# Performance work log

Measured on AMD Instinct MI355X. Metric: run time of the kernel, lower is better.

## Reference

```python
import jax, jax.numpy as jnp
import numpy as np

N, E, D_IN, HID, HEADS = 50000, 800000, 128, 32, 8
NEG_SLOPE = 0.2


def gat_conv(x, src, dst, W_src, W_dst, a_src, a_dst, b, heads, ch, concat):
    n = x.shape[0]
    hs = (x @ W_src).reshape(n, heads, ch)  # source-side features [N,H,C]
    hd = (x @ W_dst).reshape(n, heads, ch)  # dest-side features   [N,H,C]
    alpha_s = jnp.einsum('nhc,hc->nh', hs, a_src)  # [N,H]
    alpha_d = jnp.einsum('nhc,hc->nh', hd, a_dst)  # [N,H]
    e = jax.nn.leaky_relu(alpha_s[src] + alpha_d[dst], NEG_SLOPE)  # [E,H]
    # segment softmax over edges grouped by destination node
    m = jax.ops.segment_max(e, dst, num_segments=n)
    m = jnp.where(jnp.isfinite(m), m, 0.0)
    e = jnp.exp(e - jax.lax.stop_gradient(m)[dst])
    denom = jax.ops.segment_sum(e, dst, num_segments=n)
    alpha = e / (denom[dst] + 1e-16)  # [E,H]
    # weighted scatter-aggregate of source features to destinations
    out = jax.ops.segment_sum(hs[src] * alpha[:, :, None], dst, num_segments=n)  # [N,H,C]
    out = out.reshape(n, heads * ch) if concat else out.mean(axis=1)
    return out + b


def setup_inputs() -> dict:
    key = jax.random.key(0)
    ks = jax.random.split(key, 12)
    glorot = lambda k, shape: jax.random.normal(k, shape, jnp.float32) * np.sqrt(2.0 / (shape[0] + shape[-1]))
    x = jax.random.normal(ks[0], (N, D_IN), jnp.float32)
    edge_index = jax.random.randint(ks[1], (2, E), 0, N, jnp.int64)
    return {
        'x': x,
        'edge_index': edge_index,
        'W1_src': glorot(ks[2], (D_IN, HEADS * HID)),
        'W1_dst': glorot(ks[3], (D_IN, HEADS * HID)),
        'a1_src': glorot(ks[4], (HEADS, HID)),
        'a1_dst': glorot(ks[5], (HEADS, HID)),
        'b1': jnp.zeros((HEADS * HID,), jnp.float32),
        'W2_src': glorot(ks[6], (HEADS * HID, HID)),
        'W2_dst': glorot(ks[7], (HEADS * HID, HID)),
        'a2_src': glorot(ks[8], (1, HID)),
        'a2_dst': glorot(ks[9], (1, HID)),
        'b2': jnp.zeros((HID,), jnp.float32),
    }


def reference(x, edge_index, W1_src, W1_dst, a1_src, a1_dst, b1,
              W2_src, W2_dst, a2_src, a2_dst, b2):
    src, dst = edge_index[0], edge_index[1]
    h = gat_conv(x, src, dst, W1_src, W1_dst, a1_src, a1_dst, b1, HEADS, HID, True)
    h = jax.nn.relu(h)
    out = gat_conv(h, src, dst, W2_src, W2_dst, a2_src, a2_dst, b2, 1, HID, True)
    return out
```

## Files before the change

### kernel.cpp

```cpp
#include <hip/hip_runtime.h>
#include <hip/hip_bf16.h>

#define NEG_SLOPE 0.2f

typedef unsigned int uint;
typedef unsigned short ushort;
typedef __attribute__((ext_vector_type(8))) short short8;
typedef __attribute__((ext_vector_type(4))) float floatx4;

static __device__ __forceinline__ ushort f2bf(float f) {
    uint u = __float_as_uint(f);
    uint r = (u + 0x7fffu + ((u >> 16) & 1u)) >> 16;
    return (ushort)r;
}
static __device__ __forceinline__ float bf2f(uint s) {
    return __uint_as_float(s << 16);
}

__global__ __launch_bounds__(256) void histprep_kernel(
    const int* __restrict__ dst, int* __restrict__ deg, int E, int HB,
    const float* __restrict__ W1_src, const float* __restrict__ W2_src,
    const float* __restrict__ W1_dst, const float* __restrict__ a1_dst,
    const float* __restrict__ W2_dst, const float* __restrict__ a2_dst,
    ushort* __restrict__ W1t, ushort* __restrict__ W2t,
    float* __restrict__ wc1, float* __restrict__ wc2) {
    if (blockIdx.x < (uint)HB) {
        int i = blockIdx.x * blockDim.x + threadIdx.x;
        int e0 = i * 2;
        if (e0 + 1 < E) {
            int2 d2 = ((const int2*)dst)[i];
            atomicAdd(&deg[d2.x], 1);
            atomicAdd(&deg[d2.y], 1);
        } else if (e0 < E) {
            atomicAdd(&deg[dst[e0]], 1);
        }
        return;
    }
    int i = (blockIdx.x - HB) * blockDim.x + threadIdx.x;
    if (i < 32768) {
        int nc = i & 255, k = i >> 8;
        W1t[nc * 128 + k] = f2bf(W1_src[k * 256 + nc]);
    } else if (i < 32768 + 8192) {
        int i2 = i - 32768;
        int c = i2 & 31, k = i2 >> 5;
        W2t[c * 256 + k] = f2bf(W2_src[k * 32 + c]);
    } else if (i < 32768 + 8192 + 1024) {
        int i3 = i - 32768 - 8192;
        int k = i3 >> 3, h = i3 & 7;
        float s = 0.f;
#pragma unroll
        for (int c = 0; c < 32; ++c)
            s += W1_dst[k * 256 + h * 32 + c] * a1_dst[h * 32 + c];
        wc1[i3] = s;
    } else if (i < 32768 + 8192 + 1024 + 256) {
        int k = i - 32768 - 8192 - 1024;
        float s = 0.f;
#pragma unroll
        for (int c = 0; c < 32; ++c)
            s += W2_dst[k * 32 + c] * a2_dst[c];
        wc2[k] = s;
    }
}

__global__ __launch_bounds__(256) void scanrs_kernel(
    const int* __restrict__ deg, int* __restrict__ rs,
    int* __restrict__ cursor, int* __restrict__ agg,
    int* __restrict__ flag, int n, int E) {
    __shared__ int sh[256];
    int tid = threadIdx.x;
    int c = blockIdx.x;
    int i = c * 256 + tid;
    int d = (i < n) ? deg[i] : 0;
    sh[tid] = d;
    __syncthreads();
    for (int off = 1; off < 256; off <<= 1) {
        int t = (tid >= off) ? sh[tid - off] : 0;
        __syncthreads();
        sh[tid] += t;
        __syncthreads();
    }
    int incl = sh[tid];
    if (tid == 255) {
        agg[c] = incl;
        __threadfence();
        __hip_atomic_store(&flag[c], 1, __ATOMIC_RELEASE,
                           __HIP_MEMORY_SCOPE_AGENT);
    }
    int vt = 0;
    if (tid < c) {
        while (__hip_atomic_load(&flag[tid], __ATOMIC_ACQUIRE,
                                 __HIP_MEMORY_SCOPE_AGENT) == 0) {}
        vt = agg[tid];
    }
    __syncthreads();
    sh[tid] = vt;
    __syncthreads();
    for (int off = 128; off > 0; off >>= 1) {
        if (tid < off) sh[tid] += sh[tid + off];
        __syncthreads();
    }
    int boff = sh[0];
    if (i < n) {
        int v = incl - d + boff;
        rs[i] = v;
        cursor[i] = v;
    }
    if (c == 0 && tid == 0) rs[n] = E;
}

__global__ __launch_bounds__(256) void fill_kernel(
    const int* __restrict__ src, const int* __restrict__ dst,
    int* __restrict__ cursor, int* __restrict__ csr_src, int E) {
    int i = blockIdx.x * blockDim.x + threadIdx.x;
    int e0 = i * 2;
    if (e0 + 1 < E) {
        int2 d2 = ((const int2*)dst)[i];
        int2 s2 = ((const int2*)src)[i];
        int p0 = atomicAdd(&cursor[d2.x], 1);
        int p1 = atomicAdd(&cursor[d2.y], 1);
        csr_src[p0] = s2.x;
        csr_src[p1] = s2.y;
    } else if (e0 < E) {
        int pos = atomicAdd(&cursor[dst[e0]], 1);
        csr_src[pos] = src[e0];
    }
}

__global__ __launch_bounds__(256) void gemm1_mfma(
    const float* __restrict__ x, const ushort* __restrict__ W1t,
    const float* __restrict__ a_src, const float* __restrict__ wc1,
    ushort* __restrict__ hs1b, float* __restrict__ as1,
    float* __restrict__ ad1, int n) {
    __shared__ ushort At[128 * 128];
    __shared__ ushort Out[128 * 128];
    int m0 = blockIdx.x * 128;
    int tid = threadIdx.x;
#pragma unroll
    for (int i = 0; i < 8; ++i) {
        int id = tid + i * 256;
        int m = id >> 4, c = id & 15;
        int gm = m0 + m;
        uint4 pk = {0, 0, 0, 0};
        if (gm < n) {
            const float4* xp = (const float4*)(x + (size_t)gm * 128 + c * 8);
            float4 v0 = xp[0], v1 = xp[1];
            pk.x = (uint)f2bf(v0.x) | ((uint)f2bf(v0.y) << 16);
            pk.y = (uint)f2bf(v0.z) | ((uint)f2bf(v0.w) << 16);
            pk.z = (uint)f2bf(v1.x) | ((uint)f2bf(v1.y) << 16);
            pk.w = (uint)f2bf(v1.z) | ((uint)f2bf(v1.w) << 16);
        }
        *(uint4*)(At + m * 128 + ((c ^ (m & 15)) * 8)) = pk;
    }
    __syncthreads();
    int wid = tid >> 6, lane = tid & 63;
    int q = lane >> 4, l16 = lane & 15;
    int wm = (wid >> 1) * 64;
    int wn = (wid & 1) * 64;
    floatx4 z = {0.f, 0.f, 0.f, 0.f};
    for (int nhalf = 0; nhalf < 2; ++nhalf) {
        int gn0 = nhalf * 128 + wn;
        floatx4 acc[4][4];
#pragma unroll
        for (int mt = 0; mt < 4; ++mt)
#pragma unroll
            for (int nt = 0; nt < 4; ++nt) acc[mt][nt] = z;
#pragma unroll
        for (int s = 0; s < 4; ++s) {
            short8 af[4], bf[4];
#pragma unroll
            for (int mt = 0; mt < 4; ++mt) {
                int row = wm + mt * 16 + l16;
                int c = s * 4 + q;
                af[mt] = *(const short8*)(At + row * 128 + ((c ^ (row & 15)) * 8));
            }
#pragma unroll
            for (int nt = 0; nt < 4; ++nt) {
                int col = gn0 + nt * 16 + l16;
                bf[nt] = *(const short8*)(W1t + col * 128 + s * 32 + q * 8);
            }
#pragma unroll
            for (int mt = 0; mt < 4; ++mt)
#pragma unroll
                for (int nt = 0; nt < 4; ++nt)
                    acc[mt][nt] = __builtin_amdgcn_mfma_f32_16x16x32_bf16(
                        af[mt], bf[nt], acc[mt][nt], 0, 0, 0);
        }
        __syncthreads();
#pragma unroll
        for (int mt = 0; mt < 4; ++mt)
#pragma unroll
            for (int nt = 0; nt < 4; ++nt) {
                floatx4 a = acc[mt][nt];
                int colL = wn + nt * 16 + l16;
#pragma unroll
                for (int r = 0; r < 4; ++r) {
                    int rowL = wm + mt * 16 + q * 4 + r;
                    Out[rowL * 128 + colL] = f2bf(a[r]);
                }
            }
        __syncthreads();
#pragma unroll
        for (int i = 0; i < 8; ++i) {
            int id = tid + i * 256;
            int m = id >> 4, c8 = id & 15;
            int gm = m0 + m;
            if (gm < n) {
                uint4 v = *(uint4*)(Out + m * 128 + c8 * 8);
                *(uint4*)(hs1b + (size_t)gm * 256 + nhalf * 128 + c8 * 8) = v;
            }
        }
#pragma unroll
        for (int i = 0; i < 2; ++i) {
            int id = tid + i * 256;
            int m = id & 127, hl = id >> 7;
            int gm = m0 + m;
            if (gm < n) {
                int h = nhalf * 4 + hl;
                const ushort* row = Out + m * 128 + hl * 32;
                const float* av = a_src + h * 32;
                float s = 0.f;
#pragma unroll
                for (int c = 0; c < 32; ++c) s += bf2f(row[c]) * av[c];
                as1[(size_t)gm * 8 + h] = s;
            }
        }
    }
#pragma unroll
    for (int i = 0; i < 4; ++i) {
        int id = tid + i * 256;
        int m = id & 127, h = id >> 7;
        int gm = m0 + m;
        if (gm < n) {
            float s = 0.f;
            for (int c = 0; c < 16; ++c) {
                const ushort* p = At + m * 128 + ((c ^ (m & 15)) * 8);
#pragma unroll
                for (int jj = 0; jj < 8; ++jj)
                    s += bf2f(p[jj]) * wc1[(c * 8 + jj) * 8 + h];
            }
            ad1[(size_t)gm * 8 + h] = s;
        }
    }
}

__global__ __launch_bounds__(256) void gather1(
    const int* __restrict__ csr_src, const int* __restrict__ rs,
    const ushort* __restrict__ hs1b, const float* __restrict__ as1,
    const float* __restrict__ ad1, const float* __restrict__ b1,
    ushort* __restrict__ h1b, int n) {
    int gid = blockIdx.x * blockDim.x + threadIdx.x;
    int node = gid >> 6;
    int lane = threadIdx.x & 63;
    if (node >= n) return;
    int j = lane >> 5, l = lane & 31;
    int h = l >> 2;
    float ad_v = ad1[node * 8 + h];
    int start = rs[node], cnt = rs[node + 1] - start;
    float acc0 = 0.f, acc1 = 0.f, acc2 = 0.f, acc3 = 0.f;
    float acc4 = 0.f, acc5 = 0.f, acc6 = 0.f, acc7 = 0.f;
    float dacc = 0.f;
    int i = j;
    for (; i + 2 < cnt; i += 4) {
        int sA = csr_src[start + i];
        int sB = csr_src[start + i + 2];
        float tA = as1[sA * 8 + h] + ad_v;
        float tB = as1[sB * 8 + h] + ad_v;
        uint4 vA = *(const uint4*)(hs1b + (size_t)sA * 256 + l * 8);
        uint4 vB = *(const uint4*)(hs1b + (size_t)sB * 256 + l * 8);
        tA = (tA >= 0.f) ? tA : NEG_SLOPE * tA;
        tB = (tB >= 0.f) ? tB : NEG_SLOPE * tB;
        float wA = __expf(tA);
        float wB = __expf(tB);
        acc0 += bf2f(vA.x & 0xffffu) * wA + bf2f(vB.x & 0xffffu) * wB;
        acc1 += bf2f(vA.x >> 16) * wA + bf2f(vB.x >> 16) * wB;
        acc2 += bf2f(vA.y & 0xffffu) * wA + bf2f(vB.y & 0xffffu) * wB;
        acc3 += bf2f(vA.y >> 16) * wA + bf2f(vB.y >> 16) * wB;
        acc4 += bf2f(vA.z & 0xffffu) * wA + bf2f(vB.z & 0xffffu) * wB;
        acc5 += bf2f(vA.z >> 16) * wA + bf2f(vB.z >> 16) * wB;
        acc6 += bf2f(vA.w & 0xffffu) * wA + bf2f(vB.w & 0xffffu) * wB;
        acc7 += bf2f(vA.w >> 16) * wA + bf2f(vB.w >> 16) * wB;
        dacc += wA + wB;
    }
    for (; i < cnt; i += 2) {
        int s = csr_src[start + i];
        float t = as1[s * 8 + h] + ad_v;
        uint4 v = *(const uint4*)(hs1b + (size_t)s * 256 + l * 8);
        t = (t >= 0.f) ? t : NEG_SLOPE * t;
        float w = __expf(t);
        acc0 += bf2f(v.x & 0xffffu) * w;
        acc1 += bf2f(v.x >> 16) * w;
        acc2 += bf2f(v.y & 0xffffu) * w;
        acc3 += bf2f(v.y >> 16) * w;
        acc4 += bf2f(v.z & 0xffffu) * w;
        acc5 += bf2f(v.z >> 16) * w;
        acc6 += bf2f(v.w & 0xffffu) * w;
        acc7 += bf2f(v.w >> 16) * w;
        dacc += w;
    }
    acc0 += __shfl_xor(acc0, 32, 64);
    acc1 += __shfl_xor(acc1, 32, 64);
    acc2 += __shfl_xor(acc2, 32, 64);
    acc3 += __shfl_xor(acc3, 32, 64);
    acc4 += __shfl_xor(acc4, 32, 64);
    acc5 += __shfl_xor(acc5, 32, 64);
    acc6 += __shfl_xor(acc6, 32, 64);
    acc7 += __shfl_xor(acc7, 32, 64);
    dacc += __shfl_xor(dacc, 32, 64);
    if (j == 0) {
        float inv = 1.f / (dacc + 1e-16f);
        float4 b0 = ((const float4*)b1)[l * 2];
        float4 b4 = ((const float4*)b1)[l * 2 + 1];
        float o0 = fmaxf(fmaf(acc0, inv, b0.x), 0.f);
        float o1 = fmaxf(fmaf(acc1, inv, b0.y), 0.f);
        float o2 = fmaxf(fmaf(acc2, inv, b0.z), 0.f);
        float o3 = fmaxf(fmaf(acc3, inv, b0.w), 0.f);
        float o4 = fmaxf(fmaf(acc4, inv, b4.x), 0.f);
        float o5 = fmaxf(fmaf(acc5, inv, b4.y), 0.f);
        float o6 = fmaxf(fmaf(acc6, inv, b4.z), 0.f);
        float o7 = fmaxf(fmaf(acc7, inv, b4.w), 0.f);
        uint4 pk;
        pk.x = (uint)f2bf(o0) | ((uint)f2bf(o1) << 16);
        pk.y = (uint)f2bf(o2) | ((uint)f2bf(o3) << 16);
        pk.z = (uint)f2bf(o4) | ((uint)f2bf(o5) << 16);
        pk.w = (uint)f2bf(o6) | ((uint)f2bf(o7) << 16);
        *(uint4*)(h1b + (size_t)node * 256 + l * 8) = pk;
    }
}

__global__ __launch_bounds__(256) void gemm2_mfma(
    const ushort* __restrict__ h1b, const ushort* __restrict__ W2t,
    const float* __restrict__ a2_src, const float* __restrict__ wc2,
    ushort* __restrict__ hs2b, float* __restrict__ as2,
    float* __restrict__ ad2, int n) {
    __shared__ ushort At[128 * 256];
    __shared__ ushort Out[128 * 32];
    int m0 = blockIdx.x * 128;
    int tid = threadIdx.x;
#pragma unroll
    for (int i = 0; i < 16; ++i) {
        int id = tid + i * 256;
        int m = id >> 5, c = id & 31;
        int gm = m0 + m;
        uint4 v = {0, 0, 0, 0};
        if (gm < n) v = *(const uint4*)(h1b + (size_t)gm * 256 + c * 8);
        *(uint4*)(At + m * 256 + ((c ^ (m & 15)) * 8)) = v;
    }
    __syncthreads();
    int wid = tid >> 6, lane = tid & 63;
    int q = lane >> 4, l16 = lane & 15;
    int wm = wid * 32;
    floatx4 z = {0.f, 0.f, 0.f, 0.f};
    floatx4 acc[2][2] = {{z, z}, {z, z}};
#pragma unroll
    for (int s = 0; s < 8; ++s) {
        short8 af[2], bf[2];
#pragma unroll
        for (int mt = 0; mt < 2; ++mt) {
            int row = wm + mt * 16 + l16;
            int c = s * 4 + q;
            af[mt] = *(const short8*)(At + row * 256 + ((c ^ (row & 15)) * 8));
        }
#pragma unroll
        for (int nt = 0; nt < 2; ++nt) {
            int col = nt * 16 + l16;
            bf[nt] = *(const short8*)(W2t + col * 256 + s * 32 + q * 8);
        }
#pragma unroll
        for (int mt = 0; mt < 2; ++mt)
#pragma unroll
            for (int nt = 0; nt < 2; ++nt)
                acc[mt][nt] = __builtin_amdgcn_mfma_f32_16x16x32_bf16(
                    af[mt], bf[nt], acc[mt][nt], 0, 0, 0);
    }
#pragma unroll
    for (int mt = 0; mt < 2; ++mt)
#pragma unroll
        for (int nt = 0; nt < 2; ++nt) {
            floatx4 a = acc[mt][nt];
            int colL = nt * 16 + l16;
#pragma unroll
            for (int r = 0; r < 4; ++r) {
                int rowL = wm + mt * 16 + q * 4 + r;
                Out[rowL * 32 + colL] = f2bf(a[r]);
            }
        }
    __syncthreads();
#pragma unroll
    for (int i = 0; i < 2; ++i) {
        int id = tid + i * 256;
        int c4 = id & 3, m = id >> 2;
        int gm = m0 + m;
        if (gm < n)
            *(uint4*)(hs2b + (size_t)gm * 32 + c4 * 8) =
                *(uint4*)(Out + m * 32 + c4 * 8);
    }
    if (tid < 128) {
        int gm = m0 + tid;
        if (gm < n) {
            float s = 0.f;
#pragma unroll
            for (int c2 = 0; c2 < 32; ++c2)
                s += bf2f(Out[tid * 32 + c2]) * a2_src[c2];
            as2[gm] = s;
        }
    } else {
        int m = tid - 128, gm = m0 + m;
        if (gm < n) {
            float s = 0.f;
            for (int c = 0; c < 32; ++c) {
                const ushort* p = At + m * 256 + ((c ^ (m & 15)) * 8);
#pragma unroll
                for (int jj = 0; jj < 8; ++jj)
                    s += bf2f(p[jj]) * wc2[c * 8 + jj];
            }
            ad2[gm] = s;
        }
    }
}

__global__ __launch_bounds__(256) void gather2(
    const int* __restrict__ csr_src, const int* __restrict__ rs,
    const ushort* __restrict__ hs2b, const float* __restrict__ as2,
    const float* __restrict__ ad2, const float* __restrict__ b2,
    float* __restrict__ out, int n) {
    int gid = blockIdx.x * blockDim.x + threadIdx.x;
    int node = gid >> 6;
    int lane = threadIdx.x & 63;
    if (node >= n) return;
    int g = lane >> 3, l = lane & 7;
    float ad_v = ad2[node];
    int start = rs[node], cnt = rs[node + 1] - start;
    float a0 = 0.f, a1 = 0.f, a2 = 0.f, a3 = 0.f, dacc = 0.f;
    for (int i = g; i < cnt; i += 8) {
        int s = csr_src[start + i];
        float t = as2[s] + ad_v;
        t = (t >= 0.f) ? t : NEG_SLOPE * t;
        float w = __expf(t);
        uint2 v = *(const uint2*)(hs2b + (size_t)s * 32 + l * 4);
        a0 += bf2f(v.x & 0xffffu) * w;
        a1 += bf2f(v.x >> 16) * w;
        a2 += bf2f(v.y & 0xffffu) * w;
        a3 += bf2f(v.y >> 16) * w;
        dacc += w;
    }
#pragma unroll
    for (int m = 8; m <= 32; m <<= 1) {
        a0 += __shfl_xor(a0, m, 64);
        a1 += __shfl_xor(a1, m, 64);
        a2 += __shfl_xor(a2, m, 64);
        a3 += __shfl_xor(a3, m, 64);
        dacc += __shfl_xor(dacc, m, 64);
    }
    if (g == 0) {
        float inv = 1.f / (dacc + 1e-16f);
        float4 bv = ((const float4*)b2)[l];
        float4 o;
        o.x = fmaf(a0, inv, bv.x);
        o.y = fmaf(a1, inv, bv.y);
        o.z = fmaf(a2, inv, bv.z);
        o.w = fmaf(a3, inv, bv.w);
        *(float4*)(out + (size_t)node * 32 + l * 4) = o;
    }
}

extern "C" void kernel_launch(void* const* d_in, const int* in_sizes, int n_in,
                              void* d_out, int out_size, void* d_ws, size_t ws_size,
                              hipStream_t stream) {
    const float* x      = (const float*)d_in[0];
    const int*   eidx   = (const int*)d_in[1];
    const float* W1_src = (const float*)d_in[2];
    const float* W1_dst = (const float*)d_in[3];
    const float* a1_src = (const float*)d_in[4];
    const float* a1_dst = (const float*)d_in[5];
    const float* b1     = (const float*)d_in[6];
    const float* W2_src = (const float*)d_in[7];
    const float* W2_dst = (const float*)d_in[8];
    const float* a2_src = (const float*)d_in[9];
    const float* a2_dst = (const float*)d_in[10];
    const float* b2     = (const float*)d_in[11];

    const int n = in_sizes[0] / 128;
    const int E = in_sizes[1] / 2;
    const int* srcp = eidx;
    const int* dstp = eidx + E;
    const int nb = (n + 255) / 256;

    char* ws = (char*)d_ws;
    size_t o = 0;
    auto alloc = [&](size_t bytes) {
        void* p = ws + o;
        o += (bytes + 255) & ~(size_t)255;
        return p;
    };
    ushort* W1t  = (ushort*)alloc(256 * 128 * 2);
    ushort* W2t  = (ushort*)alloc(32 * 256 * 2);
    ushort* hs1b = (ushort*)alloc((size_t)n * 256 * 2);
    ushort* h1b  = (ushort*)alloc((size_t)n * 256 * 2);
    ushort* hs2b = (ushort*)alloc((size_t)n * 32 * 2);
    float* as1 = (float*)alloc((size_t)n * 8 * 4);
    float* ad1 = (float*)alloc((size_t)n * 8 * 4);
    float* as2 = (float*)alloc((size_t)n * 4);
    float* ad2 = (float*)alloc((size_t)n * 4);
    float* wc1 = (float*)alloc(1024 * 4);
    float* wc2 = (float*)alloc(256 * 4);
    int* csrmeta = (int*)alloc(((size_t)n + 512) * 4);
    int* deg  = csrmeta;
    int* agg  = csrmeta + n;
    int* flag = csrmeta + n + 256;
    int* rs      = (int*)alloc(((size_t)n + 1) * 4);
    int* cursor  = (int*)alloc((size_t)n * 4);
    int* csr_src = (int*)alloc((size_t)E * 4);

    hipMemsetAsync(csrmeta, 0, ((size_t)n + 512) * sizeof(int), stream);

    const int HB = (E / 2 + 255) / 256;
    const int PB = (32768 + 8192 + 1024 + 256 + 255) / 256;
    histprep_kernel<<<HB + PB, 256, 0, stream>>>(
        dstp, deg, E, HB, W1_src, W2_src, W1_dst, a1_dst, W2_dst, a2_dst,
        W1t, W2t, wc1, wc2);
    scanrs_kernel<<<nb, 256, 0, stream>>>(deg, rs, cursor, agg, flag, n, E);
    fill_kernel<<<(E / 2 + 255) / 256, 256, 0, stream>>>(srcp, dstp, cursor,
                                                         csr_src, E);

    gemm1_mfma<<<(n + 127) / 128, 256, 0, stream>>>(
        x, W1t, a1_src, wc1, hs1b, as1, ad1, n);
    gather1<<<(n + 3) / 4, 256, 0, stream>>>(
        csr_src, rs, hs1b, as1, ad1, b1, h1b, n);

    gemm2_mfma<<<(n + 127) / 128, 256, 0, stream>>>(
        h1b, W2t, a2_src, wc2, hs2b, as2, ad2, n);
    gather2<<<(n + 3) / 4, 256, 0, stream>>>(
        csr_src, rs, hs2b, as2, ad2, b2, (float*)d_out, n);
}
```

Baseline: 323.4 us.

## Fold attention projections into GEMM weights and split gemm1 over column halves

```diff
diff --git a/kernel.cpp b/kernel.cpp
--- a/kernel.cpp
+++ b/kernel.cpp
@@ -19,11 +19,11 @@
 
 __global__ __launch_bounds__(256) void histprep_kernel(
     const int* __restrict__ dst, int* __restrict__ deg, int E, int HB,
-    const float* __restrict__ W1_src, const float* __restrict__ W2_src,
+    const float* __restrict__ W1_src, const float* __restrict__ a1_src,
     const float* __restrict__ W1_dst, const float* __restrict__ a1_dst,
+    const float* __restrict__ W2_src, const float* __restrict__ a2_src,
     const float* __restrict__ W2_dst, const float* __restrict__ a2_dst,
-    ushort* __restrict__ W1t, ushort* __restrict__ W2t,
-    float* __restrict__ wc1, float* __restrict__ wc2) {
+    ushort* __restrict__ W1e, ushort* __restrict__ W2e) {
     if (blockIdx.x < (uint)HB) {
         int i = blockIdx.x * blockDim.x + threadIdx.x;
         int e0 = i * 2;
@@ -39,26 +39,35 @@
     int i = (blockIdx.x - HB) * blockDim.x + threadIdx.x;
     if (i < 32768) {
         int nc = i & 255, k = i >> 8;
-        W1t[nc * 128 + k] = f2bf(W1_src[k * 256 + nc]);
-    } else if (i < 32768 + 8192) {
-        int i2 = i - 32768;
-        int c = i2 & 31, k = i2 >> 5;
-        W2t[c * 256 + k] = f2bf(W2_src[k * 32 + c]);
-    } else if (i < 32768 + 8192 + 1024) {
-        int i3 = i - 32768 - 8192;
-        int k = i3 >> 3, h = i3 & 7;
+        W1e[nc * 128 + k] = f2bf(W1_src[k * 256 + nc]);
+    } else if (i < 34816) {
+        int j = i - 32768;
+        int h = (j >> 7) & 7, k = j & 127;
+        bool is_ws = j < 1024;
+        const float* W = is_ws ? W1_src : W1_dst;
+        const float* a = is_ws ? a1_src : a1_dst;
         float s = 0.f;
 #pragma unroll
         for (int c = 0; c < 32; ++c)
-            s += W1_dst[k * 256 + h * 32 + c] * a1_dst[h * 32 + c];
-        wc1[i3] = s;
-    } else if (i < 32768 + 8192 + 1024 + 256) {
-        int k = i - 32768 - 8192 - 1024;
+            s += W[k * 256 + h * 32 + c] * a[h * 32 + c];
+        W1e[((is_ws ? 256 : 264) + h) * 128 + k] = f2bf(s);
+    } else if (i < 34816 + 8192) {
+        int j = i - 34816;
+        int c = j & 31, k = j >> 5;
+        W2e[c * 256 + k] = f2bf(W2_src[k * 32 + c]);
+    } else if (i < 34816 + 8192 + 512) {
+        int j = i - 34816 - 8192;
+        int k = j & 255;
+        bool is_ws = j < 256;
+        const float* W = is_ws ? W2_src : W2_dst;
+        const float* a = is_ws ? a2_src : a2_dst;
         float s = 0.f;
 #pragma unroll
-        for (int c = 0; c < 32; ++c)
-            s += W2_dst[k * 32 + c] * a2_dst[c];
-        wc2[k] = s;
+        for (int c = 0; c < 32; ++c) s += W[k * 32 + c] * a[c];
+        W2e[(is_ws ? 32 : 33) * 256 + k] = f2bf(s);
+    } else if (i < 34816 + 8192 + 512 + 3584) {
+        int j = i - 34816 - 8192 - 512;
+        W2e[34 * 256 + j] = 0;
     }
 }
 
@@ -127,13 +136,13 @@
 }
 
 __global__ __launch_bounds__(256) void gemm1_mfma(
-    const float* __restrict__ x, const ushort* __restrict__ W1t,
-    const float* __restrict__ a_src, const float* __restrict__ wc1,
+    const float* __restrict__ x, const ushort* __restrict__ W1e,
     ushort* __restrict__ hs1b, float* __restrict__ as1,
     float* __restrict__ ad1, int n) {
     __shared__ ushort At[128 * 128];
     __shared__ ushort Out[128 * 128];
-    int m0 = blockIdx.x * 128;
+    int mblk = blockIdx.x >> 1, nhalf = blockIdx.x & 1;
+    int m0 = mblk * 128;
     int tid = threadIdx.x;
 #pragma unroll
     for (int i = 0; i < 8; ++i) {
@@ -156,89 +165,79 @@
     int q = lane >> 4, l16 = lane & 15;
     int wm = (wid >> 1) * 64;
     int wn = (wid & 1) * 64;
+    int gn0 = nhalf * 128 + wn;
+    bool do_e = (nhalf == 0) && ((wid & 1) == 0);
     floatx4 z = {0.f, 0.f, 0.f, 0.f};
-    for (int nhalf = 0; nhalf < 2; ++nhalf) {
-        int gn0 = nhalf * 128 + wn;
-        floatx4 acc[4][4];
+    floatx4 acc[4][4];
+    floatx4 acc_e[4] = {z, z, z, z};
+#pragma unroll
+    for (int mt = 0; mt < 4; ++mt)
+#pragma unroll
+        for (int nt = 0; nt < 4; ++nt) acc[mt][nt] = z;
+#pragma unroll
+    for (int s = 0; s < 4; ++s) {
+        short8 af[4], bf[4];
+#pragma unroll
+        for (int mt = 0; mt < 4; ++mt) {
+            int row = wm + mt * 16 + l16;
+            int c = s * 4 + q;
+            af[mt] = *(const short8*)(At + row * 128 + ((c ^ (row & 15)) * 8));
+        }
+#pragma unroll
+        for (int nt = 0; nt < 4; ++nt) {
+            int col = gn0 + nt * 16 + l16;
+            bf[nt] = *(const short8*)(W1e + col * 128 + s * 32 + q * 8);
+        }
 #pragma unroll
         for (int mt = 0; mt < 4; ++mt)
 #pragma unroll
-            for (int nt = 0; nt < 4; ++nt) acc[mt][nt] = z;
-#pragma unroll
-        for (int s = 0; s < 4; ++s) {
-            short8 af[4], bf[4];
-#pragma unroll
-            for (int mt = 0; mt < 4; ++mt) {
-                int row = wm + mt * 16 + l16;
-                int c = s * 4 + q;
-                af[mt] = *(const short8*)(At + row * 128 + ((c ^ (row & 15)) * 8));
+            for (int nt = 0; nt < 4; ++nt)
+                acc[mt][nt] = __builtin_amdgcn_mfma_f32_16x16x32_bf16(
+                    af[mt], bf[nt], acc[mt][nt], 0, 0, 0);
+        if (do_e) {
+            short8 bfe = *(const short8*)(W1e + (256 + l16) * 128 + s * 32 + q * 8);
+#pragma unroll
+            for (int mt = 0; mt < 4; ++mt)
+                acc_e[mt] = __builtin_amdgcn_mfma_f32_16x16x32_bf16(
+                    af[mt], bfe, acc_e[mt], 0, 0, 0);
+        }
+    }
+#pragma unroll
+    for (int mt = 0; mt < 4; ++mt)
+#pragma unroll
+        for (int nt = 0; nt < 4; ++nt) {
+            floatx4 a = acc[mt][nt];
+            int colL = wn + nt * 16 + l16;
+#pragma unroll
+            for (int r = 0; r < 4; ++r) {
+                int rowL = wm + mt * 16 + q * 4 + r;
+                Out[rowL * 128 + (((colL >> 3) ^ (rowL & 15)) * 8) + (colL & 7)]
+                    = f2bf(a[r]);
             }
-#pragma unroll
-            for (int nt = 0; nt < 4; ++nt) {
-                int col = gn0 + nt * 16 + l16;
-                bf[nt] = *(const short8*)(W1t + col * 128 + s * 32 + q * 8);
-            }
-#pragma unroll
-            for (int mt = 0; mt < 4; ++mt)
-#pragma unroll
-                for (int nt = 0; nt < 4; ++nt)
-                    acc[mt][nt] = __builtin_amdgcn_mfma_f32_16x16x32_bf16(
-                        af[mt], bf[nt], acc[mt][nt], 0, 0, 0);
-        }
-        __syncthreads();
-#pragma unroll
-        for (int mt = 0; mt < 4; ++mt)
-#pragma unroll
-            for (int nt = 0; nt < 4; ++nt) {
-                floatx4 a = acc[mt][nt];
-                int colL = wn + nt * 16 + l16;
-#pragma unroll
-                for (int r = 0; r < 4; ++r) {
-                    int rowL = wm + mt * 16 + q * 4 + r;
-                    Out[rowL * 128 + colL] = f2bf(a[r]);
+        }
+    if (do_e) {
+#pragma unroll
+        for (int mt = 0; mt < 4; ++mt) {
+            floatx4 ae = acc_e[mt];
+#pragma unroll
+            for (int r = 0; r < 4; ++r) {
+                int gm = m0 + wm + mt * 16 + q * 4 + r;
+                if (gm < n) {
+                    if (l16 < 8) as1[(size_t)gm * 8 + l16] = ae[r];
+                    else         ad1[(size_t)gm * 8 + l16 - 8] = ae[r];
                 }
             }
-        __syncthreads();
-#pragma unroll
-        for (int i = 0; i < 8; ++i) {
-            int id = tid + i * 256;
-            int m = id >> 4, c8 = id & 15;
-            int gm = m0 + m;
-            if (gm < n) {
-                uint4 v = *(uint4*)(Out + m * 128 + c8 * 8);
-                *(uint4*)(hs1b + (size_t)gm * 256 + nhalf * 128 + c8 * 8) = v;
-            }
-        }
-#pragma unroll
-        for (int i = 0; i < 2; ++i) {
-            int id = tid + i * 256;
-            int m = id & 127, hl = id >> 7;
-            int gm = m0 + m;
-            if (gm < n) {
-                int h = nhalf * 4 + hl;
-                const ushort* row = Out + m * 128 + hl * 32;
-                const float* av = a_src + h * 32;
-                float s = 0.f;
-#pragma unroll
-                for (int c = 0; c < 32; ++c) s += bf2f(row[c]) * av[c];
-                as1[(size_t)gm * 8 + h] = s;
-            }
-        }
-    }
-#pragma unroll
-    for (int i = 0; i < 4; ++i) {
+        }
+    }
+    __syncthreads();
+#pragma unroll
+    for (int i = 0; i < 8; ++i) {
         int id = tid + i * 256;
-        int m = id & 127, h = id >> 7;
+        int m = id >> 4, c8 = id & 15;
         int gm = m0 + m;
         if (gm < n) {
-            float s = 0.f;
-            for (int c = 0; c < 16; ++c) {
-                const ushort* p = At + m * 128 + ((c ^ (m & 15)) * 8);
-#pragma unroll
-                for (int jj = 0; jj < 8; ++jj)
-                    s += bf2f(p[jj]) * wc1[(c * 8 + jj) * 8 + h];
-            }
-            ad1[(size_t)gm * 8 + h] = s;
+            uint4 v = *(uint4*)(Out + m * 128 + ((c8 ^ (m & 15)) * 8));
+            *(uint4*)(hs1b + (size_t)gm * 256 + nhalf * 128 + c8 * 8) = v;
         }
     }
 }
@@ -328,8 +327,7 @@
 }
 
 __global__ __launch_bounds__(256) void gemm2_mfma(
-    const ushort* __restrict__ h1b, const ushort* __restrict__ W2t,
-    const float* __restrict__ a2_src, const float* __restrict__ wc2,
+    const ushort* __restrict__ h1b, const ushort* __restrict__ W2e,
     ushort* __restrict__ hs2b, float* __restrict__ as2,
     float* __restrict__ ad2, int n) {
     __shared__ ushort At[128 * 256];
@@ -351,6 +349,7 @@
     int wm = wid * 32;
     floatx4 z = {0.f, 0.f, 0.f, 0.f};
     floatx4 acc[2][2] = {{z, z}, {z, z}};
+    floatx4 acc_e[2] = {z, z};
 #pragma unroll
     for (int s = 0; s < 8; ++s) {
         short8 af[2], bf[2];
@@ -363,14 +362,18 @@
 #pragma unroll
         for (int nt = 0; nt < 2; ++nt) {
             int col = nt * 16 + l16;
-            bf[nt] = *(const short8*)(W2t + col * 256 + s * 32 + q * 8);
-        }
-#pragma unroll
-        for (int mt = 0; mt < 2; ++mt)
+            bf[nt] = *(const short8*)(W2e + col * 256 + s * 32 + q * 8);
+        }
+        short8 bfe = *(const short8*)(W2e + (32 + l16) * 256 + s * 32 + q * 8);
+#pragma unroll
+        for (int mt = 0; mt < 2; ++mt) {
 #pragma unroll
             for (int nt = 0; nt < 2; ++nt)
                 acc[mt][nt] = __builtin_amdgcn_mfma_f32_16x16x32_bf16(
                     af[mt], bf[nt], acc[mt][nt], 0, 0, 0);
+            acc_e[mt] = __builtin_amdgcn_mfma_f32_16x16x32_bf16(
+                af[mt], bfe, acc_e[mt], 0, 0, 0);
+        }
     }
 #pragma unroll
     for (int mt = 0; mt < 2; ++mt)
@@ -381,9 +384,22 @@
 #pragma unroll
             for (int r = 0; r < 4; ++r) {
                 int rowL = wm + mt * 16 + q * 4 + r;
-                Out[rowL * 32 + colL] = f2bf(a[r]);
+                Out[rowL * 32 + (((colL >> 3) ^ (rowL & 3)) * 8) + (colL & 7)]
+                    = f2bf(a[r]);
             }
         }
+#pragma unroll
+    for (int mt = 0; mt < 2; ++mt) {
+        floatx4 ae = acc_e[mt];
+#pragma unroll
+        for (int r = 0; r < 4; ++r) {
+            int gm = m0 + wm + mt * 16 + q * 4 + r;
+            if (gm < n) {
+                if (l16 == 0) as2[gm] = ae[r];
+                else if (l16 == 1) ad2[gm] = ae[r];
+            }
+        }
+    }
     __syncthreads();
 #pragma unroll
     for (int i = 0; i < 2; ++i) {
@@ -392,29 +408,7 @@
         int gm = m0 + m;
         if (gm < n)
             *(uint4*)(hs2b + (size_t)gm * 32 + c4 * 8) =
-                *(uint4*)(Out + m * 32 + c4 * 8);
-    }
-    if (tid < 128) {
-        int gm = m0 + tid;
-        if (gm < n) {
-            float s = 0.f;
-#pragma unroll
-            for (int c2 = 0; c2 < 32; ++c2)
-                s += bf2f(Out[tid * 32 + c2]) * a2_src[c2];
-            as2[gm] = s;
-        }
-    } else {
-        int m = tid - 128, gm = m0 + m;
-        if (gm < n) {
-            float s = 0.f;
-            for (int c = 0; c < 32; ++c) {
-                const ushort* p = At + m * 256 + ((c ^ (m & 15)) * 8);
-#pragma unroll
-                for (int jj = 0; jj < 8; ++jj)
-                    s += bf2f(p[jj]) * wc2[c * 8 + jj];
-            }
-            ad2[gm] = s;
-        }
+                *(uint4*)(Out + m * 32 + ((c4 ^ (m & 3)) * 8));
     }
 }
 
@@ -492,8 +486,8 @@
         o += (bytes + 255) & ~(size_t)255;
         return p;
     };
-    ushort* W1t  = (ushort*)alloc(256 * 128 * 2);
-    ushort* W2t  = (ushort*)alloc(32 * 256 * 2);
+    ushort* W1e  = (ushort*)alloc(272 * 128 * 2);
+    ushort* W2e  = (ushort*)alloc(48 * 256 * 2);
     ushort* hs1b = (ushort*)alloc((size_t)n * 256 * 2);
     ushort* h1b  = (ushort*)alloc((size_t)n * 256 * 2);
     ushort* hs2b = (ushort*)alloc((size_t)n * 32 * 2);
@@ -501,8 +495,6 @@
     float* ad1 = (float*)alloc((size_t)n * 8 * 4);
     float* as2 = (float*)alloc((size_t)n * 4);
     float* ad2 = (float*)alloc((size_t)n * 4);
-    float* wc1 = (float*)alloc(1024 * 4);
-    float* wc2 = (float*)alloc(256 * 4);
     int* csrmeta = (int*)alloc(((size_t)n + 512) * 4);
     int* deg  = csrmeta;
     int* agg  = csrmeta + n;
@@ -514,21 +506,21 @@
     hipMemsetAsync(csrmeta, 0, ((size_t)n + 512) * sizeof(int), stream);
 
     const int HB = (E / 2 + 255) / 256;
-    const int PB = (32768 + 8192 + 1024 + 256 + 255) / 256;
+    const int PB = (34816 + 8192 + 512 + 3584 + 255) / 256;
     histprep_kernel<<<HB + PB, 256, 0, stream>>>(
-        dstp, deg, E, HB, W1_src, W2_src, W1_dst, a1_dst, W2_dst, a2_dst,
-        W1t, W2t, wc1, wc2);
+        dstp, deg, E, HB, W1_src, a1_src, W1_dst, a1_dst,
+        W2_src, a2_src, W2_dst, a2_dst, W1e, W2e);
     scanrs_kernel<<<nb, 256, 0, stream>>>(deg, rs, cursor, agg, flag, n, E);
     fill_kernel<<<(E / 2 + 255) / 256, 256, 0, stream>>>(srcp, dstp, cursor,
                                                          csr_src, E);
 
-    gemm1_mfma<<<(n + 127) / 128, 256, 0, stream>>>(
-        x, W1t, a1_src, wc1, hs1b, as1, ad1, n);
+    gemm1_mfma<<<((n + 127) / 128) * 2, 256, 0, stream>>>(
+        x, W1e, hs1b, as1, ad1, n);
     gather1<<<(n + 3) / 4, 256, 0, stream>>>(
         csr_src, rs, hs1b, as1, ad1, b1, h1b, n);
 
     gemm2_mfma<<<(n + 127) / 128, 256, 0, stream>>>(
-        h1b, W2t, a2_src, wc2, hs2b, as2, ad2, n);
+        h1b, W2e, hs2b, as2, ad2, n);
     gather2<<<(n + 3) / 4, 256, 0, stream>>>(
         csr_src, rs, hs2b, as2, ad2, b2, (float*)d_out, n);
 }
```

Measured after the change: 316.4 us. 2.2% less time.
